# Optimization experiments

Hardware: AMD Instinct MI355X
Metric: run time of the kernel (lower is better)

Reference implementation:

```python
import jax, jax.numpy as jnp
import numpy as np

# NSA hyperparams (match init_kwargs)
KS, ST, SEL, TOPN, WIN = 32, 16, 64, 16, 512
NEG = -1e30  # additive mask value (finite so fp32 softmax stays stable)


def setup_inputs() -> dict:
    key = jax.random.key(0)
    ks = jax.random.split(key, 6)
    B, S, Hq, Hk, D, Dv = 1, 2048, 16, 2, 128, 128
    q = jax.random.normal(ks[0], (B, S, Hq, D), jnp.float32)
    k = jax.random.normal(ks[1], (B, S, Hk, D), jnp.float32)
    v = jax.random.normal(ks[2], (B, S, Hk, Dv), jnp.float32)
    # learned per-position compression weights for K and V blocks
    w_cmp_k = jax.random.normal(ks[3], (KS,), jnp.float32) / KS
    w_cmp_v = jax.random.normal(ks[4], (KS,), jnp.float32) / KS
    # gating head: Linear(qk_head_dim, 3) -> sigmoid
    w_gate = jax.random.normal(ks[5], (D, 3), jnp.float32) * 0.02
    b_gate = jnp.zeros((3,), jnp.float32)
    return dict(q=q, k=k, v=v, w_cmp_k=w_cmp_k, w_cmp_v=w_cmp_v,
                w_gate=w_gate, b_gate=b_gate)


def _nsa(q, k, v, w_cmp_k, w_cmp_v, w_gate, b_gate):
    B, S, Hq, D = q.shape
    Hk = k.shape[2]
    G = Hq // Hk                      # GQA group size
    Dv = v.shape[-1]
    scale = D ** -0.5
    t_pos = jnp.arange(S)

    # ---- 1. compressed-KV attention (CompressAttn) ----
    T = (S - KS) // ST + 1            # number of compressed blocks
    widx = jnp.arange(T)[:, None] * ST + jnp.arange(KS)[None, :]   # [T, KS]
    cmp_k = jnp.einsum('btknd,k->btnd', k[:, widx], w_cmp_k)        # [B,T,Hk,D]
    cmp_v = jnp.einsum('btknd,k->btnd', v[:, widx], w_cmp_v)        # [B,T,Hk,Dv]

    qg = q.reshape(B, S, Hk, G, D)
    s_cmp = jnp.einsum('bsngd,btnd->bngst', qg, cmp_k) * scale      # [B,Hk,G,S,T]
    blk_end = jnp.arange(T) * ST + KS - 1
    cmp_mask = blk_end[None, :] <= t_pos[:, None]                   # [S,T] block fully past
    p_cmp = jax.nn.softmax(jnp.where(cmp_mask, s_cmp, NEG), axis=-1)
    p_cmp = p_cmp * cmp_mask          # zero rows with no visible block
    cmp_o = jnp.einsum('bngst,btnd->bsngd', p_cmp, cmp_v).reshape(B, S, Hq, Dv)

    # ---- 2. top-n selection-block scoring (select_for_fwd_bwd) ----
    NSel = S // SEL
    starts = jnp.arange(T) * ST
    b_lo = starts // SEL
    b_hi = (starts + KS - 1) // SEL
    bidx = jnp.arange(NSel)
    # map compressed-block probs onto overlapping selection blocks
    Mmap = ((bidx[None, :] >= b_lo[:, None]) & (bidx[None, :] <= b_hi[:, None])).astype(q.dtype)  # [T,NSel]
    p_slc = jnp.einsum('bngst,tm->bnsm', p_cmp, Mmap)               # sum over group g -> [B,Hk,S,NSel]

    cur_blk = t_pos // SEL
    blk_causal = (bidx[None, :] * SEL) <= t_pos[:, None]            # [S,NSel]
    forced = (bidx[None, :] == 0) | (bidx[None, :] == cur_blk[:, None])
    blk_score = jnp.where(forced, -NEG, p_slc)                      # always keep block 0 + current
    blk_score = jnp.where(blk_causal, blk_score, NEG)
    vals, inds = jax.lax.top_k(blk_score, TOPN)                     # [B,Hk,S,TOPN]
    valid = (vals > NEG / 2).astype(q.dtype)
    sel_blk_mask = (jax.nn.one_hot(inds, NSel, dtype=q.dtype) * valid[..., None]).sum(-2) > 0  # [B,Hk,S,NSel]

    # ---- 3. block-sparse selected attention (select_attn) ----
    tok_sel_mask = jnp.repeat(sel_blk_mask, SEL, axis=-1)           # [B,Hk,S,S]
    causal = t_pos[None, :] <= t_pos[:, None]                       # [S,S]
    tok_sel_mask = tok_sel_mask & causal
    s_tok = jnp.einsum('bsngd,bjnd->bngsj', qg, k) * scale          # [B,Hk,G,S,S] shared scores
    p_sel = jax.nn.softmax(jnp.where(tok_sel_mask[:, :, None], s_tok, NEG), axis=-1)
    sel_o = jnp.einsum('bngsj,bjnd->bsngd', p_sel, v).reshape(B, S, Hq, Dv)

    win_mask = causal & ((t_pos[:, None] - t_pos[None, :]) <= WIN)
    p_win = jax.nn.softmax(jnp.where(win_mask, s_tok, NEG), axis=-1)
    win_o = jnp.einsum('bngsj,bjnd->bsngd', p_win, v).reshape(B, S, Hq, Dv)

    # ---- 5. learned sigmoid gating combine ----
    gate = jax.nn.sigmoid(jnp.einsum('bshd,dc->bshc', q, w_gate) + b_gate)  # [B,S,Hq,3]
    return (cmp_o * gate[..., 0:1] + sel_o * gate[..., 1:2] + win_o * gate[..., 2:3])


def reference(q, k, v, w_cmp_k, w_cmp_v, w_gate, b_gate):
    return _nsa(q, k, v, w_cmp_k, w_cmp_v, w_gate, b_gate)
```

## Files before the change

kernel.cpp:

```cpp
#include <hip/hip_runtime.h>

#define SS   2048
#define HQ   16
#define HK   2
#define GQ   8
#define DD   128
#define DV   128
#define KS   32
#define ST   16
#define SELB 64
#define TOPN 16
#define WINW 512
#define TT   127
#define NSEL 32
#define QSC  0.12751744f

typedef __attribute__((ext_vector_type(8))) short bf16x8;
typedef __attribute__((ext_vector_type(4))) float f32x4;

#if defined(__has_builtin)
#  if __has_builtin(__builtin_amdgcn_exp2f)
#    define EXP2(x) __builtin_amdgcn_exp2f(x)
#  endif
#endif
#ifndef EXP2
#  define EXP2(x) __expf((x) * 0.6931471805599453f)
#endif

__device__ __forceinline__ short f2bf(float x) {
    union { float f; unsigned u; } a; a.f = x;
    unsigned r = a.u + 0x7FFFu + ((a.u >> 16) & 1u);
    return (short)(r >> 16);
}
__device__ __forceinline__ float bf2f(short b) {
    union { unsigned u; float f; } x; x.u = ((unsigned)(unsigned short)b) << 16; return x.f;
}

__global__ __launch_bounds__(256) void k_prep(
    const float* __restrict__ k, const float* __restrict__ v,
    const float* __restrict__ wck, const float* __restrict__ wcv,
    short* __restrict__ kfr, short* __restrict__ vfr,
    short* __restrict__ ckh, short* __restrict__ ckl,
    short* __restrict__ cvfr)
{
    __shared__ float red[256];
    int bid = blockIdx.x, tid = threadIdx.x;
    int lane = tid & 63, quad = (lane >> 4) & 3, l16 = lane & 15;
    if (bid < 256) {
        int tb = bid >> 1, n = bid & 1;
        int kb = tid >> 6;
        int token = tb * 16 + l16;
        int feat = kb * 32 + quad * 8;
        const float* src = &k[(token * HK + n) * DD + feat];
        bf16x8 t;
        #pragma unroll
        for (int e = 0; e < 8; ++e) t[e] = f2bf(src[e]);
        *(bf16x8*)&kfr[(((n * 128 + tb) * 4 + kb) * 64 + lane) * 8] = t;
    } else if (bid < 512) {
        int id = bid - 256;
        int cb = id >> 3, n = (id >> 2) & 1, it = id & 3;
        int frag = it * 4 + (tid >> 6);
        int h = frag >> 3, f = frag & 7;
        int d = f * 16 + l16;
        int tok0 = cb * 64 + h * 32 + quad * 8;
        bf16x8 t;
        #pragma unroll
        for (int e = 0; e < 8; ++e) t[e] = f2bf(v[((tok0 + e) * HK + n) * DV + d]);
        *(bf16x8*)&vfr[((((n * 32 + cb) * 2 + h) * 8 + f) * 64 + lane) * 8] = t;
    } else if (bid < 768) {
        int id = bid - 512;
        int n = id & 1, t = id >> 1;
        int d = tid & 127, jh = tid >> 7;
        float a = 0.f;
        if (t < TT) {
            #pragma unroll
            for (int jj = 0; jj < 16; ++jj) {
                int j = jh * 16 + jj;
                a += k[((t * ST + j) * HK + n) * DD + d] * wck[j];
            }
        }
        red[tid] = a;
        __syncthreads();
        if (tid < 128) {
            float s = red[tid] + red[tid + 128];
            short hi = f2bf(s);
            short lo = f2bf(s - bf2f(hi));
            int tile = t >> 4, l16i = t & 15;
            int kb = d >> 5, qd = (d >> 3) & 3, e = d & 7;
            int off = (((n * 8 + tile) * 4 + kb) * 64 + qd * 16 + l16i) * 8 + e;
            ckh[off] = hi;
            ckl[off] = lo;
        }
    } else {
        int id = bid - 768;
        int n = id & 1, tok = id >> 1;
        int d = tid & 127, jh = tid >> 7;
        float a = 0.f;
        if (tok < TT) {
            #pragma unroll
            for (int jj = 0; jj < 16; ++jj) {
                int j = jh * 16 + jj;
                a += v[((tok * ST + j) * HK + n) * DV + d] * wcv[j];
            }
        }
        red[tid] = a;
        __syncthreads();
        if (tid < 128) {
            float s = red[tid] + red[tid + 128];
            int w2 = d >> 5, half = (d >> 4) & 1, l16i = d & 15;
            int kb = tok >> 5, qd = (tok >> 3) & 3, e = tok & 7;
            cvfr[((((n * 4 + w2) * 2 + half) * 4 + kb) * 64 + qd * 16 + l16i) * 8 + e] = f2bf(s);
        }
    }
}

__global__ __launch_bounds__(256, 4) void k_fused(
    const float* __restrict__ q,
    const short* __restrict__ ckh, const short* __restrict__ ckl,
    const short* __restrict__ cvfr,
    const short* __restrict__ kfr, const short* __restrict__ vfr,
    const float* __restrict__ wg, const float* __restrict__ bg,
    float* __restrict__ out)
{
    int s0 = (SS - 2) - (int)blockIdx.x * 2;
    int s1 = s0 + 1;
    int n = blockIdx.y;
    int tid = threadIdx.x;
    int w = tid >> 6, lane = tid & 63, quad = lane >> 4, l16 = lane & 15;

    __shared__ union {
        struct {
            float qs[16][132];
            float p[16][132];
            short Pt[16][136];
        } c;
        struct {
            union {
                short Pw[4][16][64];
                float o_lds[2][16][132];
            } pf;
            short OselB[16][128];
        } f;
    } u;
    __shared__ short cmpO[16][136];
    __shared__ float g3v[16][3];
    __shared__ float pslc2[2][NSEL];
    __shared__ float lw[4][16];
    __shared__ unsigned selMask[2];
    __shared__ unsigned ublk[NSEL];
    __shared__ int shUCnt;

    f32x4 z4 = {0.f, 0.f, 0.f, 0.f};
    const bf16x8 ones8 = {0x3F80, 0x3F80, 0x3F80, 0x3F80, 0x3F80, 0x3F80, 0x3F80, 0x3F80};

    for (int i = tid; i < 16 * 128; i += 256) {
        int row = i >> 7, d = i & 127;
        u.c.qs[row][d] = q[((s0 + (row >> 3)) * HQ + n * GQ + (row & 7)) * DD + d];
    }
    __syncthreads();

    bf16x8 qb[4];
    bf16x8 qlb[4];
    {
        const float* qp = &u.c.qs[l16][quad * 8];
        #pragma unroll
        for (int kb = 0; kb < 4; ++kb) {
            f32x4 x = *(const f32x4*)(qp + kb * 32);
            f32x4 y = *(const f32x4*)(qp + kb * 32 + 4);
            bf16x8 th, tl;
            #pragma unroll
            for (int j = 0; j < 4; ++j) {
                float xs = x[j] * QSC, ys = y[j] * QSC;
                th[j] = f2bf(xs);     tl[j] = f2bf(xs - bf2f(th[j]));
                th[4+j] = f2bf(ys);   tl[4+j] = f2bf(ys - bf2f(th[4+j]));
            }
            qb[kb] = th; qlb[kb] = tl;
        }
    }
    for (int tile = w; tile < 8; tile += 4) {
        const short* khp = &ckh[((n * 8 + tile) * 256 + lane) * 8];
        const short* klp = &ckl[((n * 8 + tile) * 256 + lane) * 8];
        f32x4 acc = z4;
        #pragma unroll
        for (int kb = 0; kb < 4; ++kb) {
            bf16x8 ah = *(const bf16x8*)(khp + kb * 512);
            bf16x8 al = *(const bf16x8*)(klp + kb * 512);
            acc = __builtin_amdgcn_mfma_f32_16x16x32_bf16(ah, qb[kb], acc, 0, 0, 0);
            acc = __builtin_amdgcn_mfma_f32_16x16x32_bf16(al, qb[kb], acc, 0, 0, 0);
            acc = __builtin_amdgcn_mfma_f32_16x16x32_bf16(ah, qlb[kb], acc, 0, 0, 0);
        }
        *(f32x4*)&u.c.p[l16][tile * 16 + quad * 4] = acc;
    }
    __syncthreads();

    int ntt0 = (s0 >= KS - 1) ? min((s0 - (KS - 1)) / ST + 1, TT) : 0;
    int ntt1 = (s1 >= KS - 1) ? min((s1 - (KS - 1)) / ST + 1, TT) : 0;

    #pragma unroll
    for (int rr = 0; rr < 4; ++rr) {
        int row = w * 4 + rr;
        int ntt = (row < 8) ? ntt0 : ntt1;
        int t1 = lane, t2 = lane + 64;
        float v1 = (t1 < ntt) ? u.c.p[row][t1] : -1e30f;
        float v2 = (t2 < ntt) ? u.c.p[row][t2] : -1e30f;
        float m = fmaxf(v1, v2);
        #pragma unroll
        for (int o = 32; o > 0; o >>= 1) m = fmaxf(m, __shfl_xor(m, o, 64));
        float e1 = (t1 < ntt) ? EXP2(v1 - m) : 0.f;
        float e2 = (t2 < ntt) ? EXP2(v2 - m) : 0.f;
        float ssum = e1 + e2;
        #pragma unroll
        for (int o = 32; o > 0; o >>= 1) ssum += __shfl_xor(ssum, o, 64);
        float inv = (ntt > 0) ? (1.f / ssum) : 0.f;
        e1 *= inv; e2 *= inv;
        u.c.p[row][t1] = e1; u.c.p[row][t2] = e2;
        u.c.Pt[row][t1] = f2bf(e1); u.c.Pt[row][t2] = f2bf(e2);
    }
    __syncthreads();

    if (tid < 64) {
        int p01 = tid >> 5, m = tid & 31;
        float a = 0.f;
        for (int dt = -1; dt < 4; ++dt) {
            int t = 4 * m + dt;
            if (t < 0 || t >= TT) continue;
            bool maps = (t / 4 == m) || ((t % 4 == 3) && (t / 4 == m - 1));
            if (!maps) continue;
            for (int g = 0; g < GQ; ++g) a += u.c.p[p01 * 8 + g][t];
        }
        pslc2[p01][m] = a;
    }
    __syncthreads();

    if (w < 2) {
        int p01 = w;
        int sp = p01 ? s1 : s0;
        int cur = sp / SELB;
        float v;
        if (lane < NSEL) {
            int m = lane;
            if (m == 0 || m == cur) v = 1e30f;
            else if (m * SELB <= sp) v = pslc2[p01][m];
            else v = -1e30f;
        } else v = -1e31f;
        unsigned msk = 0;
        #pragma unroll
        for (int pick = 0; pick < TOPN; ++pick) {
            float bv = v;
            #pragma unroll
            for (int o = 32; o > 0; o >>= 1) bv = fmaxf(bv, __shfl_xor(bv, o, 64));
            unsigned long long b = __ballot(v == bv);
            int best = __ffsll((long long)b) - 1;
            if (bv > -5e29f) msk |= 1u << best;
            if (lane == best) v = -1e31f;
        }
        if (lane == 0) selMask[p01] = msk;
    }
    {
        f32x4 o0 = z4, o1 = z4;
        int d0 = w * 32 + l16;
        const short* cvp = &cvfr[((n * 4 + w) * 512 + lane) * 8];
        #pragma unroll
        for (int kb = 0; kb < 4; ++kb) {
            bf16x8 pa = *(const bf16x8*)&u.c.Pt[l16][kb * 32 + quad * 8];
            bf16x8 vb0 = *(const bf16x8*)(cvp + kb * 512);
            bf16x8 vb1 = *(const bf16x8*)(cvp + 2048 + kb * 512);
            o0 = __builtin_amdgcn_mfma_f32_16x16x32_bf16(pa, vb0, o0, 0, 0, 0);
            o1 = __builtin_amdgcn_mfma_f32_16x16x32_bf16(pa, vb1, o1, 0, 0, 0);
        }
        #pragma unroll
        for (int r = 0; r < 4; ++r) {
            int h2 = quad * 4 + r;
            cmpO[h2][d0]      = f2bf(o0[r]);
            cmpO[h2][d0 + 16] = f2bf(o1[r]);
        }
    }
    __syncthreads();

    float* gpart = &u.c.p[0][0];
    if (tid == 0) {
        unsigned m0 = selMask[0], m1 = selMask[1], mu = m0 | m1;
        int uc = 0;
        for (int b = 0; b < NSEL; ++b)
            if ((mu >> b) & 1u)
                ublk[uc++] = (unsigned)(b * SELB) | (((m0 >> b) & 1u) << 30) | (((m1 >> b) & 1u) << 31);
        shUCnt = uc;
    } else if (tid >= 64) {
        int t2 = tid - 64;
        int h2 = t2 / 12, rem = t2 % 12;
        int c = rem >> 2, qtr = rem & 3;
        const float* qrow = &u.c.qs[h2][qtr * 32];
        float a = 0.f;
        #pragma unroll
        for (int d2 = 0; d2 < 32; ++d2) a += qrow[d2] * wg[(qtr * 32 + d2) * 3 + c];
        gpart[t2] = a;
    }
    __syncthreads();
    if (tid < 48) {
        int h2 = tid / 3, c = tid % 3;
        int base = h2 * 12 + c * 4;
        float a = gpart[base] + gpart[base + 1] + gpart[base + 2] + gpart[base + 3] + bg[c];
        g3v[h2][c] = 1.f / (1.f + __expf(-a));
    }
    int uCnt = shUCnt;
    int j00 = (s0 >= WINW) ? (s0 - WINW) : 0;
    int j01 = (s1 >= WINW) ? (s1 - WINW) : 0;
    int tb0 = j00 & ~63;
    int nBlkB = ((s1 - tb0) >> 6) + 1;

    int sLim = (l16 < 8) ? s0 : s1;
    f32x4 o[8];
    f32x4 lacc;

    char* pwRow = (char*)&u.f.pf.Pw[w][l16][0];
    int swz = l16 & 7;

    auto run_chunks = [&](int nB, bool selMode) {
        #pragma unroll
        for (int f = 0; f < 8; ++f) o[f] = z4;
        lacc = z4;
        int loWin = selMode ? 0 : ((l16 < 8) ? j00 : j01);
        for (int bi = w; bi < nB; bi += 4) {
            int tstart, vis;
            if (selMode) {
                unsigned e = ublk[bi];
                tstart = (int)(e & 0x0FFFFFFFu);
                vis = (l16 < 8) ? (int)((e >> 30) & 1u) : (int)(e >> 31);
            } else {
                tstart = tb0 + bi * 64;
                vis = 1;
            }
            f32x4 a4[4] = {z4, z4, z4, z4};
            {
                const short* kp = &kfr[((n * 128 + (tstart >> 4)) * 256 + lane) * 8];
                bf16x8 kf[2][4];
                #pragma unroll
                for (int t2 = 0; t2 < 2; ++t2)
                    #pragma unroll
                    for (int kb = 0; kb < 4; ++kb)
                        kf[t2][kb] = *(const bf16x8*)(kp + (t2 * 4 + kb) * 512);
                #pragma unroll
                for (int kb = 0; kb < 4; ++kb) {
                    a4[0] = __builtin_amdgcn_mfma_f32_16x16x32_bf16(kf[0][kb], qb[kb], a4[0], 0, 0, 0);
                    a4[1] = __builtin_amdgcn_mfma_f32_16x16x32_bf16(kf[1][kb], qb[kb], a4[1], 0, 0, 0);
                }
                #pragma unroll
                for (int t2 = 0; t2 < 2; ++t2)
                    #pragma unroll
                    for (int kb = 0; kb < 4; ++kb)
                        kf[t2][kb] = *(const bf16x8*)(kp + ((2 + t2) * 4 + kb) * 512);
                #pragma unroll
                for (int kb = 0; kb < 4; ++kb) {
                    a4[2] = __builtin_amdgcn_mfma_f32_16x16x32_bf16(kf[0][kb], qb[kb], a4[2], 0, 0, 0);
                    a4[3] = __builtin_amdgcn_mfma_f32_16x16x32_bf16(kf[1][kb], qb[kb], a4[3], 0, 0, 0);
                }
            }
            const short* vp = &vfr[((n * 32 + (tstart >> 6)) * 1024 + lane) * 8];
            bf16x8 vf[8];
            #pragma unroll
            for (int f = 0; f < 8; ++f) vf[f] = *(const bf16x8*)(vp + f * 512);
            {
                int lo = loWin - tstart;
                int hi = vis ? (sLim - tstart) : (lo - 1);
                int rngS = hi - lo + 1;
                unsigned rng = (unsigned)(rngS > 0 ? rngS : 0);
                int tb = quad * 4 - lo;
                #pragma unroll
                for (int tile = 0; tile < 4; ++tile) {
                    float ev[4];
                    #pragma unroll
                    for (int r = 0; r < 4; ++r) {
                        unsigned uu = (unsigned)(tb + tile * 16 + r);
                        float ex = EXP2(a4[tile][r]);
                        ev[r] = (uu < rng) ? ex : 0.f;
                    }
                    unsigned plo = (__float_as_uint(ev[1]) & 0xFFFF0000u) | (__float_as_uint(ev[0]) >> 16);
                    unsigned phi = (__float_as_uint(ev[3]) & 0xFFFF0000u) | (__float_as_uint(ev[2]) >> 16);
                    uint2 pk; pk.x = plo; pk.y = phi;
                    int chunk = (tile * 2 + (quad >> 1)) ^ swz;
                    *(uint2*)(pwRow + chunk * 16 + (quad & 1) * 8) = pk;
                }
            }
            __builtin_amdgcn_s_waitcnt(0xC07F);
            bf16x8 pa0 = *(const bf16x8*)(pwRow + ((quad ^ swz) * 16));
            bf16x8 pa1 = *(const bf16x8*)(pwRow + (((4 + quad) ^ swz) * 16));
            lacc = __builtin_amdgcn_mfma_f32_16x16x32_bf16(pa0, ones8, lacc, 0, 0, 0);
            lacc = __builtin_amdgcn_mfma_f32_16x16x32_bf16(pa1, ones8, lacc, 0, 0, 0);
            #pragma unroll
            for (int f = 0; f < 8; ++f)
                o[f] = __builtin_amdgcn_mfma_f32_16x16x32_bf16(pa0, vf[f], o[f], 0, 0, 0);
            #pragma unroll
            for (int f = 0; f < 8; ++f)
                o[f] = __builtin_amdgcn_mfma_f32_16x16x32_bf16(pa1, *(const bf16x8*)(vp + (8 + f) * 512), o[f], 0, 0, 0);
        }
    };

    auto combine = [&](bool isA) {
        if (l16 == 0) {
            #pragma unroll
            for (int r = 0; r < 4; ++r) lw[w][quad * 4 + r] = lacc[r];
        }
        __syncthreads();
        if (w >= 2) {
            #pragma unroll
            for (int f = 0; f < 8; ++f)
                #pragma unroll
                for (int r = 0; r < 4; ++r)
                    u.f.pf.o_lds[w - 2][quad * 4 + r][l16 + 16 * f] = o[f][r];
        }
        __syncthreads();
        float ltot = lw[0][l16] + lw[1][l16] + lw[2][l16] + lw[3][l16];
        float linv = 1.f / ltot;
        float linvr[4];
        #pragma unroll
        for (int r = 0; r < 4; ++r) linvr[r] = __shfl(linv, quad * 4 + r, 64);
        if (w < 2) {
            #pragma unroll
            for (int f = 0; f < 8; ++f)
                #pragma unroll
                for (int r = 0; r < 4; ++r)
                    o[f][r] += u.f.pf.o_lds[w][quad * 4 + r][l16 + 16 * f];
        }
        __syncthreads();
        if (w == 1) {
            #pragma unroll
            for (int f = 0; f < 8; ++f)
                #pragma unroll
                for (int r = 0; r < 4; ++r)
                    u.f.pf.o_lds[0][quad * 4 + r][l16 + 16 * f] = o[f][r];
        }
        __syncthreads();
        if (w == 0) {
            #pragma unroll
            for (int f = 0; f < 8; ++f)
                #pragma unroll
                for (int r = 0; r < 4; ++r)
                    o[f][r] += u.f.pf.o_lds[0][quad * 4 + r][l16 + 16 * f];
            if (isA) {
                #pragma unroll
                for (int f = 0; f < 8; ++f)
                    #pragma unroll
                    for (int r = 0; r < 4; ++r)
                        u.f.OselB[quad * 4 + r][l16 + 16 * f] = f2bf(o[f][r] * linvr[r]);
            } else {
                #pragma unroll
                for (int f = 0; f < 8; ++f)
                    #pragma unroll
                    for (int r = 0; r < 4; ++r) {
                        int h2 = quad * 4 + r;
                        int p = h2 >> 3, g = h2 & 7;
                        int d = l16 + 16 * f;
                        int ob = ((s0 + p) * HQ + n * GQ + g) * DV + d;
                        float owin = o[f][r] * linvr[r];
                        out[ob] = g3v[h2][0] * bf2f(cmpO[h2][d]) + g3v[h2][1] * bf2f(u.f.OselB[h2][d]) + g3v[h2][2] * owin;
                    }
            }
        }
        __syncthreads();
    };

    run_chunks(uCnt, true);
    combine(true);
    run_chunks(nBlkB, false);
    combine(false);
}

extern "C" void kernel_launch(void* const* d_in, const int* in_sizes, int n_in,
                              void* d_out, int out_size, void* d_ws, size_t ws_size,
                              hipStream_t stream) {
    const float* q   = (const float*)d_in[0];
    const float* k   = (const float*)d_in[1];
    const float* v   = (const float*)d_in[2];
    const float* wck = (const float*)d_in[3];
    const float* wcv = (const float*)d_in[4];
    const float* wg  = (const float*)d_in[5];
    const float* bg  = (const float*)d_in[6];
    float* out = (float*)d_out;

    short* kfr  = (short*)d_ws;
    short* vfr  = kfr + 2 * 128 * 4 * 64 * 8;
    short* ckh  = vfr + 2 * 32 * 2 * 8 * 64 * 8;
    short* ckl  = ckh + 2 * 8 * 4 * 64 * 8;
    short* cvfr = ckl + 2 * 8 * 4 * 64 * 8;

    k_prep<<<1024, 256, 0, stream>>>(k, v, wck, wcv, kfr, vfr, ckh, ckl, cvfr);
    k_fused<<<dim3(SS / 2, HK), 256, 0, stream>>>(q, ckh, ckl, cvfr, kfr, vfr, wg, bg, out);
}
```

Before: 168.0 us.

## Shrink LDS footprint and compute gate via MFMA to raise occupancy

Cuts the fused kernel's shared memory so more blocks can sit on each CU, and raises launch bounds from 4 to 8 blocks. Q is now loaded from global straight into registers instead of staged in LDS. The bf16 copy of the compressed probabilities is dropped and rebuilt from fp32 on the fly. The cross-wave output reduction is split into two halves to halve its buffer. The gating projection moves from a scalar LDS dot product to split-bf16 MFMAs against weight fragments built in the prep kernel. Risks include register spilling under the tighter launch bound and extra barriers in the halved reduction.

```diff
diff --git a/kernel.cpp b/kernel.cpp
--- a/kernel.cpp
+++ b/kernel.cpp
@@ -39,9 +39,10 @@
 __global__ __launch_bounds__(256) void k_prep(
     const float* __restrict__ k, const float* __restrict__ v,
     const float* __restrict__ wck, const float* __restrict__ wcv,
+    const float* __restrict__ wg,
     short* __restrict__ kfr, short* __restrict__ vfr,
     short* __restrict__ ckh, short* __restrict__ ckl,
-    short* __restrict__ cvfr)
+    short* __restrict__ cvfr, short* __restrict__ wgh, short* __restrict__ wgl)
 {
     __shared__ float red[256];
     int bid = blockIdx.x, tid = threadIdx.x;
@@ -91,7 +92,7 @@
             ckh[off] = hi;
             ckl[off] = lo;
         }
-    } else {
+    } else if (bid < 1024) {
         int id = bid - 768;
         int n = id & 1, tok = id >> 1;
         int d = tid & 127, jh = tid >> 7;
@@ -111,15 +112,28 @@
             int kb = tok >> 5, qd = (tok >> 3) & 3, e = tok & 7;
             cvfr[((((n * 4 + w2) * 2 + half) * 4 + kb) * 64 + qd * 16 + l16i) * 8 + e] = f2bf(s);
         }
+    } else {
+        int kb = tid >> 6;
+        bf16x8 th, tl;
+        #pragma unroll
+        for (int e = 0; e < 8; ++e) {
+            int kidx = kb * 32 + quad * 8 + e;
+            float x = (l16 < 3) ? wg[kidx * 3 + l16] : 0.f;
+            th[e] = f2bf(x);
+            tl[e] = f2bf(x - bf2f(th[e]));
+        }
+        *(bf16x8*)&wgh[(kb * 64 + lane) * 8] = th;
+        *(bf16x8*)&wgl[(kb * 64 + lane) * 8] = tl;
     }
 }
 
-__global__ __launch_bounds__(256, 4) void k_fused(
+__global__ __launch_bounds__(256, 8) void k_fused(
     const float* __restrict__ q,
     const short* __restrict__ ckh, const short* __restrict__ ckl,
     const short* __restrict__ cvfr,
     const short* __restrict__ kfr, const short* __restrict__ vfr,
-    const float* __restrict__ wg, const float* __restrict__ bg,
+    const short* __restrict__ wgh, const short* __restrict__ wgl,
+    const float* __restrict__ bg,
     float* __restrict__ out)
 {
     int s0 = (SS - 2) - (int)blockIdx.x * 2;
@@ -129,19 +143,11 @@
     int w = tid >> 6, lane = tid & 63, quad = lane >> 4, l16 = lane & 15;
 
     __shared__ union {
-        struct {
-            float qs[16][132];
-            float p[16][132];
-            short Pt[16][136];
-        } c;
-        struct {
-            union {
-                short Pw[4][16][64];
-                float o_lds[2][16][132];
-            } pf;
-            short OselB[16][128];
-        } f;
+        float p[16][132];
+        short Pw[4][16][64];
+        float o2[2][16][68];
     } u;
+    __shared__ short OselB[16][128];
     __shared__ short cmpO[16][136];
     __shared__ float g3v[16][3];
     __shared__ float pslc2[2][NSEL];
@@ -153,20 +159,14 @@
     f32x4 z4 = {0.f, 0.f, 0.f, 0.f};
     const bf16x8 ones8 = {0x3F80, 0x3F80, 0x3F80, 0x3F80, 0x3F80, 0x3F80, 0x3F80, 0x3F80};
 
-    for (int i = tid; i < 16 * 128; i += 256) {
-        int row = i >> 7, d = i & 127;
-        u.c.qs[row][d] = q[((s0 + (row >> 3)) * HQ + n * GQ + (row & 7)) * DD + d];
-    }
-    __syncthreads();
-
     bf16x8 qb[4];
     bf16x8 qlb[4];
     {
-        const float* qp = &u.c.qs[l16][quad * 8];
+        const float* qpg = &q[((s0 + (l16 >> 3)) * HQ + n * GQ + (l16 & 7)) * DD + quad * 8];
         #pragma unroll
         for (int kb = 0; kb < 4; ++kb) {
-            f32x4 x = *(const f32x4*)(qp + kb * 32);
-            f32x4 y = *(const f32x4*)(qp + kb * 32 + 4);
+            f32x4 x = *(const f32x4*)(qpg + kb * 32);
+            f32x4 y = *(const f32x4*)(qpg + kb * 32 + 4);
             bf16x8 th, tl;
             #pragma unroll
             for (int j = 0; j < 4; ++j) {
@@ -175,6 +175,24 @@
                 th[4+j] = f2bf(ys);   tl[4+j] = f2bf(ys - bf2f(th[4+j]));
             }
             qb[kb] = th; qlb[kb] = tl;
+        }
+    }
+    if (w == 0) {
+        f32x4 gacc = z4;
+        #pragma unroll
+        for (int kb = 0; kb < 4; ++kb) {
+            bf16x8 wh = *(const bf16x8*)&wgh[(kb * 64 + lane) * 8];
+            bf16x8 wl = *(const bf16x8*)&wgl[(kb * 64 + lane) * 8];
+            gacc = __builtin_amdgcn_mfma_f32_16x16x32_bf16(wh, qb[kb], gacc, 0, 0, 0);
+            gacc = __builtin_amdgcn_mfma_f32_16x16x32_bf16(wl, qb[kb], gacc, 0, 0, 0);
+            gacc = __builtin_amdgcn_mfma_f32_16x16x32_bf16(wh, qlb[kb], gacc, 0, 0, 0);
+        }
+        if (quad == 0) {
+            #pragma unroll
+            for (int r = 0; r < 3; ++r) {
+                float a = gacc[r] * (1.f / QSC) + bg[r];
+                g3v[l16][r] = 1.f / (1.f + __expf(-a));
+            }
         }
     }
     for (int tile = w; tile < 8; tile += 4) {
@@ -189,7 +207,7 @@
             acc = __builtin_amdgcn_mfma_f32_16x16x32_bf16(al, qb[kb], acc, 0, 0, 0);
             acc = __builtin_amdgcn_mfma_f32_16x16x32_bf16(ah, qlb[kb], acc, 0, 0, 0);
         }
-        *(f32x4*)&u.c.p[l16][tile * 16 + quad * 4] = acc;
+        *(f32x4*)&u.p[l16][tile * 16 + quad * 4] = acc;
     }
     __syncthreads();
 
@@ -201,8 +219,8 @@
         int row = w * 4 + rr;
         int ntt = (row < 8) ? ntt0 : ntt1;
         int t1 = lane, t2 = lane + 64;
-        float v1 = (t1 < ntt) ? u.c.p[row][t1] : -1e30f;
-        float v2 = (t2 < ntt) ? u.c.p[row][t2] : -1e30f;
+        float v1 = (t1 < ntt) ? u.p[row][t1] : -1e30f;
+        float v2 = (t2 < ntt) ? u.p[row][t2] : -1e30f;
         float m = fmaxf(v1, v2);
         #pragma unroll
         for (int o = 32; o > 0; o >>= 1) m = fmaxf(m, __shfl_xor(m, o, 64));
@@ -213,8 +231,7 @@
         for (int o = 32; o > 0; o >>= 1) ssum += __shfl_xor(ssum, o, 64);
         float inv = (ntt > 0) ? (1.f / ssum) : 0.f;
         e1 *= inv; e2 *= inv;
-        u.c.p[row][t1] = e1; u.c.p[row][t2] = e2;
-        u.c.Pt[row][t1] = f2bf(e1); u.c.Pt[row][t2] = f2bf(e2);
+        u.p[row][t1] = e1; u.p[row][t2] = e2;
     }
     __syncthreads();
 
@@ -226,7 +243,7 @@
             if (t < 0 || t >= TT) continue;
             bool maps = (t / 4 == m) || ((t % 4 == 3) && (t / 4 == m - 1));
             if (!maps) continue;
-            for (int g = 0; g < GQ; ++g) a += u.c.p[p01 * 8 + g][t];
+            for (int g = 0; g < GQ; ++g) a += u.p[p01 * 8 + g][t];
         }
         pslc2[p01][m] = a;
     }
@@ -260,9 +277,14 @@
         f32x4 o0 = z4, o1 = z4;
         int d0 = w * 32 + l16;
         const short* cvp = &cvfr[((n * 4 + w) * 512 + lane) * 8];
+        const float* prow = &u.p[l16][quad * 8];
         #pragma unroll
         for (int kb = 0; kb < 4; ++kb) {
-            bf16x8 pa = *(const bf16x8*)&u.c.Pt[l16][kb * 32 + quad * 8];
+            f32x4 x = *(const f32x4*)(prow + kb * 32);
+            f32x4 y = *(const f32x4*)(prow + kb * 32 + 4);
+            bf16x8 pa;
+            #pragma unroll
+            for (int j = 0; j < 4; ++j) { pa[j] = f2bf(x[j]); pa[4+j] = f2bf(y[j]); }
             bf16x8 vb0 = *(const bf16x8*)(cvp + kb * 512);
             bf16x8 vb1 = *(const bf16x8*)(cvp + 2048 + kb * 512);
             o0 = __builtin_amdgcn_mfma_f32_16x16x32_bf16(pa, vb0, o0, 0, 0, 0);
@@ -277,7 +299,6 @@
     }
     __syncthreads();
 
-    float* gpart = &u.c.p[0][0];
     if (tid == 0) {
         unsigned m0 = selMask[0], m1 = selMask[1], mu = m0 | m1;
         int uc = 0;
@@ -285,23 +306,8 @@
             if ((mu >> b) & 1u)
                 ublk[uc++] = (unsigned)(b * SELB) | (((m0 >> b) & 1u) << 30) | (((m1 >> b) & 1u) << 31);
         shUCnt = uc;
-    } else if (tid >= 64) {
-        int t2 = tid - 64;
-        int h2 = t2 / 12, rem = t2 % 12;
-        int c = rem >> 2, qtr = rem & 3;
-        const float* qrow = &u.c.qs[h2][qtr * 32];
-        float a = 0.f;
-        #pragma unroll
-        for (int d2 = 0; d2 < 32; ++d2) a += qrow[d2] * wg[(qtr * 32 + d2) * 3 + c];
-        gpart[t2] = a;
     }
     __syncthreads();
-    if (tid < 48) {
-        int h2 = tid / 3, c = tid % 3;
-        int base = h2 * 12 + c * 4;
-        float a = gpart[base] + gpart[base + 1] + gpart[base + 2] + gpart[base + 3] + bg[c];
-        g3v[h2][c] = 1.f / (1.f + __expf(-a));
-    }
     int uCnt = shUCnt;
     int j00 = (s0 >= WINW) ? (s0 - WINW) : 0;
     int j01 = (s1 >= WINW) ? (s1 - WINW) : 0;
@@ -312,7 +318,7 @@
     f32x4 o[8];
     f32x4 lacc;
 
-    char* pwRow = (char*)&u.f.pf.Pw[w][l16][0];
+    char* pwRow = (char*)&u.Pw[w][l16][0];
     int swz = l16 & 7;
 
     auto run_chunks = [&](int nB, bool selMode) {
@@ -401,62 +407,65 @@
             for (int r = 0; r < 4; ++r) lw[w][quad * 4 + r] = lacc[r];
         }
         __syncthreads();
-        if (w >= 2) {
-            #pragma unroll
-            for (int f = 0; f < 8; ++f)
-                #pragma unroll
-                for (int r = 0; r < 4; ++r)
-                    u.f.pf.o_lds[w - 2][quad * 4 + r][l16 + 16 * f] = o[f][r];
-        }
-        __syncthreads();
         float ltot = lw[0][l16] + lw[1][l16] + lw[2][l16] + lw[3][l16];
         float linv = 1.f / ltot;
         float linvr[4];
         #pragma unroll
         for (int r = 0; r < 4; ++r) linvr[r] = __shfl(linv, quad * 4 + r, 64);
-        if (w < 2) {
-            #pragma unroll
-            for (int f = 0; f < 8; ++f)
-                #pragma unroll
-                for (int r = 0; r < 4; ++r)
-                    o[f][r] += u.f.pf.o_lds[w][quad * 4 + r][l16 + 16 * f];
-        }
-        __syncthreads();
-        if (w == 1) {
-            #pragma unroll
-            for (int f = 0; f < 8; ++f)
-                #pragma unroll
-                for (int r = 0; r < 4; ++r)
-                    u.f.pf.o_lds[0][quad * 4 + r][l16 + 16 * f] = o[f][r];
-        }
-        __syncthreads();
-        if (w == 0) {
-            #pragma unroll
-            for (int f = 0; f < 8; ++f)
-                #pragma unroll
-                for (int r = 0; r < 4; ++r)
-                    o[f][r] += u.f.pf.o_lds[0][quad * 4 + r][l16 + 16 * f];
-            if (isA) {
-                #pragma unroll
-                for (int f = 0; f < 8; ++f)
+        #pragma unroll
+        for (int half = 0; half < 2; ++half) {
+            if (w >= 2) {
+                #pragma unroll
+                for (int f = 0; f < 4; ++f)
                     #pragma unroll
                     for (int r = 0; r < 4; ++r)
-                        u.f.OselB[quad * 4 + r][l16 + 16 * f] = f2bf(o[f][r] * linvr[r]);
-            } else {
-                #pragma unroll
-                for (int f = 0; f < 8; ++f)
-                    #pragma unroll
-                    for (int r = 0; r < 4; ++r) {
-                        int h2 = quad * 4 + r;
-                        int p = h2 >> 3, g = h2 & 7;
-                        int d = l16 + 16 * f;
-                        int ob = ((s0 + p) * HQ + n * GQ + g) * DV + d;
-                        float owin = o[f][r] * linvr[r];
-                        out[ob] = g3v[h2][0] * bf2f(cmpO[h2][d]) + g3v[h2][1] * bf2f(u.f.OselB[h2][d]) + g3v[h2][2] * owin;
-                    }
-            }
-        }
-        __syncthreads();
+                        u.o2[w - 2][quad * 4 + r][l16 + 16 * f] = o[half * 4 + f][r];
+            }
+            __syncthreads();
+            if (w < 2) {
+                #pragma unroll
+                for (int f = 0; f < 4; ++f)
+                    #pragma unroll
+                    for (int r = 0; r < 4; ++r)
+                        o[half * 4 + f][r] += u.o2[w][quad * 4 + r][l16 + 16 * f];
+            }
+            __syncthreads();
+            if (w == 1) {
+                #pragma unroll
+                for (int f = 0; f < 4; ++f)
+                    #pragma unroll
+                    for (int r = 0; r < 4; ++r)
+                        u.o2[0][quad * 4 + r][l16 + 16 * f] = o[half * 4 + f][r];
+            }
+            __syncthreads();
+            if (w == 0) {
+                #pragma unroll
+                for (int f = 0; f < 4; ++f)
+                    #pragma unroll
+                    for (int r = 0; r < 4; ++r)
+                        o[half * 4 + f][r] += u.o2[0][quad * 4 + r][l16 + 16 * f];
+                if (isA) {
+                    #pragma unroll
+                    for (int f = 0; f < 4; ++f)
+                        #pragma unroll
+                        for (int r = 0; r < 4; ++r)
+                            OselB[quad * 4 + r][l16 + 16 * (half * 4 + f)] = f2bf(o[half * 4 + f][r] * linvr[r]);
+                } else {
+                    #pragma unroll
+                    for (int f = 0; f < 4; ++f)
+                        #pragma unroll
+                        for (int r = 0; r < 4; ++r) {
+                            int h2 = quad * 4 + r;
+                            int p = h2 >> 3, g = h2 & 7;
+                            int d = l16 + 16 * (half * 4 + f);
+                            int ob = ((s0 + p) * HQ + n * GQ + g) * DV + d;
+                            float owin = o[half * 4 + f][r] * linvr[r];
+                            out[ob] = g3v[h2][0] * bf2f(cmpO[h2][d]) + g3v[h2][1] * bf2f(OselB[h2][d]) + g3v[h2][2] * owin;
+                        }
+                }
+            }
+            __syncthreads();
+        }
     };
 
     run_chunks(uCnt, true);
@@ -482,7 +491,9 @@
     short* ckh  = vfr + 2 * 32 * 2 * 8 * 64 * 8;
     short* ckl  = ckh + 2 * 8 * 4 * 64 * 8;
     short* cvfr = ckl + 2 * 8 * 4 * 64 * 8;
-
-    k_prep<<<1024, 256, 0, stream>>>(k, v, wck, wcv, kfr, vfr, ckh, ckl, cvfr);
-    k_fused<<<dim3(SS / 2, HK), 256, 0, stream>>>(q, ckh, ckl, cvfr, kfr, vfr, wg, bg, out);
+    short* wgh  = cvfr + 2 * 4 * 2 * 4 * 64 * 8;
+    short* wgl  = wgh + 4 * 64 * 8;
+
+    k_prep<<<1025, 256, 0, stream>>>(k, v, wck, wcv, wg, kfr, vfr, ckh, ckl, cvfr, wgh, wgl);
+    k_fused<<<dim3(SS / 2, HK), 256, 0, stream>>>(q, ckh, ckl, cvfr, kfr, vfr, wgh, wgl, bg, out);
 }
```

New measurement: 297.0 us. +76.8%, slower.
